# Kernel tuning notes

Hardware: AMD Instinct MI355X
Metric: run time of the kernel (lower is better)

## Reference

```python
import jax, jax.numpy as jnp
import numpy as np

B, T, D = 4, 4096, 1024
C = 8.0  # RG_LRU constant c
LOGIT_LO = float(np.log(0.9 / 0.1))    # logit(0.9)
LOGIT_HI = float(np.log(0.999 / 0.001))  # logit(0.999)


def setup_inputs() -> dict:
    key = jax.random.key(0)
    ks = jax.random.split(key, 12)
    s = 1.0 / np.sqrt(D)
    z = lambda: jnp.zeros((D,), jnp.float32)
    return {
        "x": jax.random.normal(ks[0], (B, T, D), jnp.float32),
        "g1": jnp.ones((D,), jnp.float32),
        "g2": jnp.ones((D,), jnp.float32),
        # RecurrentBlock: shared linear, kernel-1 conv, output linear
        "W_lin": jax.random.normal(ks[1], (D, D), jnp.float32) * s, "b_lin": z(),
        "W_conv": jax.random.normal(ks[2], (D, D), jnp.float32) * s, "b_conv": z(),
        "W_lin2": jax.random.normal(ks[3], (D, D), jnp.float32) * s, "b_lin2": z(),
        # RG_LRU params
        "Wa": jax.random.normal(ks[4], (D, D), jnp.float32) * s, "ba": z(),
        "Wx": jax.random.normal(ks[5], (D, D), jnp.float32) * s, "bx": z(),
        "Lam": jax.random.uniform(ks[6], (D,), jnp.float32, LOGIT_LO, LOGIT_HI),
        # GatedMLPBlock
        "W1": jax.random.normal(ks[7], (D, D), jnp.float32) * s, "b1": z(),
        "W2": jax.random.normal(ks[8], (D, D), jnp.float32) * s, "b2": z(),
        "W3": jax.random.normal(ks[9], (D, D), jnp.float32) * s, "b3": z(),
    }


def rms_norm(x, g):
    # F.normalize(x, dim=-1) * sqrt(d) * g
    n = jnp.maximum(jnp.linalg.norm(x, axis=-1, keepdims=True), 1e-12)
    return (x / n) * (x.shape[-1] ** 0.5) * g


def rg_lru(x, Wa, ba, Wx, bx, Lam):
    # x: [B, T, D]
    rt = jax.nn.sigmoid(jnp.einsum('btd,hd->bth', x, Wa) + ba)
    it = jax.nn.sigmoid(jnp.einsum('btd,hd->bth', x, Wx) + bx)
    log_a = -jax.nn.softplus(-Lam)          # [D]
    a = jnp.exp(log_a * rt / C)             # [B, T, D]
    gated = jnp.sqrt(1.0 - a * a) * (it * x)

    def step(h, ag):
        at, gt = ag
        h = at * h + gt
        return h, h

    h0 = jnp.zeros((x.shape[0], x.shape[2]), x.dtype)
    _, hs = jax.lax.scan(step, h0, (jnp.swapaxes(a, 0, 1), jnp.swapaxes(gated, 0, 1)))
    return jnp.swapaxes(hs, 0, 1)           # [B, T, D]


def reference(x, g1, g2, W_lin, b_lin, W_conv, b_conv, W_lin2, b_lin2,
              Wa, ba, Wx, bx, Lam, W1, b1, W2, b2, W3, b3):
    residual = x
    xn = rms_norm(x, g1)

    # RecurrentBlock (note: same linear used for both branches, as in source)
    lin = xn @ W_lin.T + b_lin
    x_gel = jax.nn.gelu(lin, approximate=False)
    x_rg = lin @ W_conv.T + b_conv          # Conv1d kernel_size=1 == pointwise linear
    x_rg = rg_lru(x_rg, Wa, ba, Wx, bx, Lam)
    xr = (x_gel * x_rg) @ W_lin2.T + b_lin2

    residual = xr + residual
    xm = rms_norm(residual, g2)

    # GatedMLPBlock
    out = jax.nn.sigmoid(xm @ W1.T + b1)
    gate = jax.nn.gelu(out, approximate=False)
    combined = gate * (xm @ W2.T + b2)
    y = combined @ W3.T + b3
    return y + residual
```

## Files before the change

kernel.cpp:

```cpp
#include <hip/hip_runtime.h>
#include <cstdint>
#include <cstddef>

typedef unsigned short u16;
typedef __attribute__((ext_vector_type(8))) __bf16 bf16x8;
typedef __attribute__((ext_vector_type(4))) float f32x4;

#define DD 1024
#define MM 16384
#define NCH 64
#define CLEN 64

__device__ __forceinline__ u16 f2b(float f) {
    uint32_t u = __float_as_uint(f);
    u += 0x7fffu + ((u >> 16) & 1u);
    return (u16)(u >> 16);
}
__device__ __forceinline__ float b2f(u16 v) {
    return __uint_as_float(((uint32_t)v) << 16);
}
__device__ __forceinline__ float sigmoid_f(float v) { return 1.f / (1.f + __expf(-v)); }
__device__ __forceinline__ float gelu_f(float v) {
    return 0.5f * v * (1.f + erff(v * 0.70710678118654752f));
}

__device__ __forceinline__ void glds16(const u16* g, u16* l) {
    __builtin_amdgcn_global_load_lds(
        (const __attribute__((address_space(1))) void*)g,
        (__attribute__((address_space(3))) void*)l, 16, 0, 0);
}

template <int MODE>
__global__ __launch_bounds__(256, 2)
void gemm_bt(const u16* __restrict__ A, const u16* __restrict__ Bw,
             const float* __restrict__ bias,
             const float* __restrict__ auxf, const u16* __restrict__ auxb,
             u16* __restrict__ outb, float* __restrict__ outf)
{
    const int K = DD, N = DD;
    __shared__ __align__(16) u16 As[128 * 32];
    __shared__ __align__(16) u16 Bs[128 * 32];

    const int tid = threadIdx.x;
    const int m0 = blockIdx.y * 128, n0 = blockIdx.x * 128;
    const int wave = tid >> 6, lane = tid & 63;
    const int wm = (wave >> 1) * 64, wn = (wave & 1) * 64;
    const int lr = lane & 15, lq = lane >> 4;

    const u16* Ag = A + (size_t)(m0 + (tid >> 2)) * K + (tid & 3) * 8;
    const u16* Bg = Bw + (size_t)(n0 + (tid >> 2)) * K + (tid & 3) * 8;
    u16* la0 = &As[tid * 8];
    u16* la1 = &As[(tid + 256) * 8];
    u16* lb0 = &Bs[tid * 8];
    u16* lb1 = &Bs[(tid + 256) * 8];

    f32x4 acc[4][4] = {};

    for (int k0 = 0; k0 < K; k0 += 32) {
        glds16(Ag + k0, la0);
        glds16(Ag + (size_t)64 * K + k0, la1);
        glds16(Bg + k0, lb0);
        glds16(Bg + (size_t)64 * K + k0, lb1);
        __syncthreads();

        bf16x8 av[4], bv[4];
#pragma unroll
        for (int i = 0; i < 4; i++)
            av[i] = *(const bf16x8*)&As[(wm + i * 16 + lr) * 32 + lq * 8];
#pragma unroll
        for (int j = 0; j < 4; j++)
            bv[j] = *(const bf16x8*)&Bs[(wn + j * 16 + lr) * 32 + lq * 8];
#pragma unroll
        for (int i = 0; i < 4; i++)
#pragma unroll
            for (int j = 0; j < 4; j++)
                acc[i][j] = __builtin_amdgcn_mfma_f32_16x16x32_bf16(
                    av[i], bv[j], acc[i][j], 0, 0, 0);
        __syncthreads();
    }

#pragma unroll
    for (int i = 0; i < 4; i++) {
        const int mrow = m0 + wm + i * 16 + lq * 4;
#pragma unroll
        for (int j = 0; j < 4; j++) {
            const int ncol = n0 + wn + j * 16 + lr;
            const float bz = bias[ncol];
#pragma unroll
            for (int p = 0; p < 4; p++) {
                const size_t idx = (size_t)(mrow + p) * N + ncol;
                float v = acc[i][j][p] + bz;
                if constexpr (MODE == 0) {
                    outb[idx] = f2b(v);
                } else if constexpr (MODE == 1) {
                    outb[idx] = f2b(sigmoid_f(v));
                } else if constexpr (MODE == 2) {
                    outf[idx] = v + auxf[idx];
                } else if constexpr (MODE == 3) {
                    outb[idx] = f2b(gelu_f(sigmoid_f(v)));
                } else if constexpr (MODE == 4) {
                    outb[idx] = f2b(b2f(auxb[idx]) * v);
                } else {
                    outf[idx] = v + auxf[idx];
                }
            }
        }
    }
}

__global__ __launch_bounds__(256)
void rmsnorm_k(const float* __restrict__ x, const float* __restrict__ g,
               u16* __restrict__ out)
{
    const int row = blockIdx.x;
    const int t = threadIdx.x;
    const float4 v = ((const float4*)(x + (size_t)row * DD))[t];
    float ss = v.x * v.x + v.y * v.y + v.z * v.z + v.w * v.w;
#pragma unroll
    for (int o = 32; o > 0; o >>= 1) ss += __shfl_down(ss, o, 64);
    __shared__ float wsum[4];
    if ((t & 63) == 0) wsum[t >> 6] = ss;
    __syncthreads();
    const float tot = wsum[0] + wsum[1] + wsum[2] + wsum[3];
    const float sc = 32.0f * rsqrtf(fmaxf(tot, 1e-24f));
    const float4 gv = ((const float4*)g)[t];
    ushort4 o4;
    o4.x = f2b(v.x * sc * gv.x);
    o4.y = f2b(v.y * sc * gv.y);
    o4.z = f2b(v.z * sc * gv.z);
    o4.w = f2b(v.w * sc * gv.w);
    ((ushort4*)(out + (size_t)row * DD))[t] = o4;
}

__global__ __launch_bounds__(256)
void conv_w(const float* __restrict__ in, u16* __restrict__ out)
{
    const int i = (blockIdx.x * 256 + threadIdx.x) * 4;
    const float4 v = *(const float4*)(in + i);
    ushort4 o;
    o.x = f2b(v.x); o.y = f2b(v.y); o.z = f2b(v.z); o.w = f2b(v.w);
    *(ushort4*)(out + i) = o;
}

__global__ __launch_bounds__(256)
void scan_chunks(const u16* __restrict__ rt, const u16* __restrict__ it,
                 const u16* __restrict__ rg, const float* __restrict__ Lam,
                 float* __restrict__ P, float* __restrict__ Hl)
{
    const int d = blockIdx.x * 256 + threadIdx.x;
    const int c = blockIdx.y, b = blockIdx.z;
    const float k = -log1pf(__expf(-Lam[d])) * 0.125f;
    const size_t base = (((size_t)b * 4096) + (size_t)c * CLEN) * DD + d;
    float p = 1.f, h = 0.f;
#pragma unroll 4
    for (int t = 0; t < CLEN; t++) {
        const size_t ix = base + (size_t)t * DD;
        const float r = b2f(rt[ix]);
        const float i = b2f(it[ix]);
        const float xv = b2f(rg[ix]);
        const float a = __expf(k * r);
        const float g = sqrtf(fmaxf(1.f - a * a, 0.f)) * (i * xv);
        p *= a;
        h = fmaf(a, h, g);
    }
    const int o = (b * NCH + c) * DD + d;
    P[o] = p;
    Hl[o] = h;
}

__global__ __launch_bounds__(256)
void scan_carry(const float* __restrict__ P, const float* __restrict__ Hl,
                float* __restrict__ Cin)
{
    const int idx = blockIdx.x * 256 + threadIdx.x;
    const int b = idx >> 10, d = idx & 1023;
    float h = 0.f;
    for (int c = 0; c < NCH; c++) {
        const int o = (b * NCH + c) * DD + d;
        Cin[o] = h;
        h = fmaf(P[o], h, Hl[o]);
    }
}

__global__ __launch_bounds__(256)
void scan_apply(const u16* __restrict__ rt, const u16* __restrict__ it,
                const u16* __restrict__ rg, const u16* __restrict__ lin,
                const float* __restrict__ Lam, const float* __restrict__ Cin,
                u16* __restrict__ yin)
{
    const int d = blockIdx.x * 256 + threadIdx.x;
    const int c = blockIdx.y, b = blockIdx.z;
    const float k = -log1pf(__expf(-Lam[d])) * 0.125f;
    const size_t base = (((size_t)b * 4096) + (size_t)c * CLEN) * DD + d;
    float h = Cin[(b * NCH + c) * DD + d];
#pragma unroll 4
    for (int t = 0; t < CLEN; t++) {
        const size_t ix = base + (size_t)t * DD;
        const float r = b2f(rt[ix]);
        const float i = b2f(it[ix]);
        const float xv = b2f(rg[ix]);
        const float a = __expf(k * r);
        const float g = sqrtf(fmaxf(1.f - a * a, 0.f)) * (i * xv);
        h = fmaf(a, h, g);
        const float l = b2f(lin[ix]);
        yin[ix] = f2b(gelu_f(l) * h);
    }
}

extern "C" void kernel_launch(void* const* d_in, const int* in_sizes, int n_in,
                              void* d_out, int out_size, void* d_ws, size_t ws_size,
                              hipStream_t stream)
{
    const float* x      = (const float*)d_in[0];
    const float* g1     = (const float*)d_in[1];
    const float* g2     = (const float*)d_in[2];
    const float* W_lin  = (const float*)d_in[3];
    const float* b_lin  = (const float*)d_in[4];
    const float* W_conv = (const float*)d_in[5];
    const float* b_conv = (const float*)d_in[6];
    const float* W_lin2 = (const float*)d_in[7];
    const float* b_lin2 = (const float*)d_in[8];
    const float* Wa     = (const float*)d_in[9];
    const float* ba     = (const float*)d_in[10];
    const float* Wx     = (const float*)d_in[11];
    const float* bx     = (const float*)d_in[12];
    const float* Lam    = (const float*)d_in[13];
    const float* W1     = (const float*)d_in[14];
    const float* b1     = (const float*)d_in[15];
    const float* W2     = (const float*)d_in[16];
    const float* b2     = (const float*)d_in[17];
    const float* W3     = (const float*)d_in[18];
    const float* b3     = (const float*)d_in[19];
    float* out = (float*)d_out;

    char* p = (char*)d_ws;
    auto alloc = [&](size_t bytes) -> char* {
        char* q = p;
        p += (bytes + 255) & ~(size_t)255;
        return q;
    };
    const size_t MD = (size_t)MM * DD;
    u16* wbf[8];
    for (int i = 0; i < 8; i++) wbf[i] = (u16*)alloc((size_t)DD * DD * 2);
    u16* t0 = (u16*)alloc(MD * 2);
    u16* t1 = (u16*)alloc(MD * 2);
    u16* t2 = (u16*)alloc(MD * 2);
    u16* t3 = (u16*)alloc(MD * 2);
    u16* t4 = (u16*)alloc(MD * 2);
    float* res2 = (float*)alloc(MD * 4);
    float* P   = (float*)alloc((size_t)4 * NCH * DD * 4);
    float* Hl  = (float*)alloc((size_t)4 * NCH * DD * 4);
    float* Cin = (float*)alloc((size_t)4 * NCH * DD * 4);

    const float* wsrc[8] = {W_lin, W_conv, Wa, Wx, W_lin2, W1, W2, W3};
    for (int i = 0; i < 8; i++)
        conv_w<<<(DD * DD) / 1024, 256, 0, stream>>>(wsrc[i], wbf[i]);

    const dim3 gg(DD / 128, MM / 128);
    const dim3 sg(DD / 256, NCH, 4);

    rmsnorm_k<<<MM, 256, 0, stream>>>(x, g1, t0);
    gemm_bt<0><<<gg, 256, 0, stream>>>(t0, wbf[0], b_lin, nullptr, nullptr, t1, nullptr);
    gemm_bt<0><<<gg, 256, 0, stream>>>(t1, wbf[1], b_conv, nullptr, nullptr, t2, nullptr);
    gemm_bt<1><<<gg, 256, 0, stream>>>(t2, wbf[2], ba, nullptr, nullptr, t0, nullptr);
    gemm_bt<1><<<gg, 256, 0, stream>>>(t2, wbf[3], bx, nullptr, nullptr, t3, nullptr);
    scan_chunks<<<sg, 256, 0, stream>>>(t0, t3, t2, Lam, P, Hl);
    scan_carry<<<4096 / 256, 256, 0, stream>>>(P, Hl, Cin);
    scan_apply<<<sg, 256, 0, stream>>>(t0, t3, t2, t1, Lam, Cin, t4);
    gemm_bt<2><<<gg, 256, 0, stream>>>(t4, wbf[4], b_lin2, x, nullptr, nullptr, res2);
    rmsnorm_k<<<MM, 256, 0, stream>>>(res2, g2, t0);
    gemm_bt<3><<<gg, 256, 0, stream>>>(t0, wbf[5], b1, nullptr, nullptr, t1, nullptr);
    gemm_bt<4><<<gg, 256, 0, stream>>>(t0, wbf[6], b2, nullptr, t1, t2, nullptr);
    gemm_bt<5><<<gg, 256, 0, stream>>>(t2, wbf[7], b3, res2, nullptr, nullptr, out);
}
```

Measured before the change: 711.7 us.

## Fuse paired GEMMs, swizzle LDS and tile order, stage bf16 epilogues through LDS

Two GEMMs that read the same input (Wa/Wx gates, and W1/W2 in the MLP) are merged into one dual-B kernel, so the A tile is loaded once and the intermediate gate tensor no longer goes through global memory. The LDS layout gets an XOR swizzle on the k-chunk to reduce bank conflicts. A 1D grid with grouped tile ordering improves L2 reuse. The bf16 epilogues are staged through padded LDS so global stores are coalesced 16-byte writes, and the eight weight-conversion launches become one. The dual kernel doubles accumulator registers, which may lower occupancy.

Result: faster. 654.6 us (-8.0%).

```diff
diff --git a/kernel.cpp b/kernel.cpp
--- a/kernel.cpp
+++ b/kernel.cpp
@@ -10,6 +10,7 @@
 #define MM 16384
 #define NCH 64
 #define CLEN 64
+#define EPAD 136
 
 __device__ __forceinline__ u16 f2b(float f) {
     uint32_t u = __float_as_uint(f);
@@ -30,29 +31,38 @@
         (__attribute__((address_space(3))) void*)l, 16, 0, 0);
 }
 
+__device__ __forceinline__ void swiz(int l, int& mt, int& nt) {
+    const int g = l >> 6, r = l & 63;
+    mt = g * 8 + (r & 7);
+    nt = r >> 3;
+}
+
 template <int MODE>
 __global__ __launch_bounds__(256, 2)
 void gemm_bt(const u16* __restrict__ A, const u16* __restrict__ Bw,
-             const float* __restrict__ bias,
-             const float* __restrict__ auxf, const u16* __restrict__ auxb,
+             const float* __restrict__ bias, const float* __restrict__ auxf,
              u16* __restrict__ outb, float* __restrict__ outf)
 {
     const int K = DD, N = DD;
-    __shared__ __align__(16) u16 As[128 * 32];
-    __shared__ __align__(16) u16 Bs[128 * 32];
-
+    __shared__ __align__(16) u16 smem[8704];
+    u16* As = smem;
+    u16* Bs = smem + 4096;
+
+    int mt, nt; swiz(blockIdx.x, mt, nt);
+    const int m0 = mt * 128, n0 = nt * 128;
     const int tid = threadIdx.x;
-    const int m0 = blockIdx.y * 128, n0 = blockIdx.x * 128;
     const int wave = tid >> 6, lane = tid & 63;
     const int wm = (wave >> 1) * 64, wn = (wave & 1) * 64;
     const int lr = lane & 15, lq = lane >> 4;
 
-    const u16* Ag = A + (size_t)(m0 + (tid >> 2)) * K + (tid & 3) * 8;
-    const u16* Bg = Bw + (size_t)(n0 + (tid >> 2)) * K + (tid & 3) * 8;
+    const int trow = tid >> 2, tcol = tid & 3;
+    const int kswz = (tcol ^ ((trow >> 1) & 3)) * 8;
+    const u16* Ag = A + (size_t)(m0 + trow) * K + kswz;
+    const u16* Bg = Bw + (size_t)(n0 + trow) * K + kswz;
     u16* la0 = &As[tid * 8];
-    u16* la1 = &As[(tid + 256) * 8];
+    u16* la1 = &As[tid * 8 + 2048];
     u16* lb0 = &Bs[tid * 8];
-    u16* lb1 = &Bs[(tid + 256) * 8];
+    u16* lb1 = &Bs[tid * 8 + 2048];
 
     f32x4 acc[4][4] = {};
 
@@ -64,12 +74,13 @@
         __syncthreads();
 
         bf16x8 av[4], bv[4];
+        const int cs = (lq ^ ((lr >> 1) & 3)) * 8;
 #pragma unroll
         for (int i = 0; i < 4; i++)
-            av[i] = *(const bf16x8*)&As[(wm + i * 16 + lr) * 32 + lq * 8];
+            av[i] = *(const bf16x8*)&As[(wm + i * 16 + lr) * 32 + cs];
 #pragma unroll
         for (int j = 0; j < 4; j++)
-            bv[j] = *(const bf16x8*)&Bs[(wn + j * 16 + lr) * 32 + lq * 8];
+            bv[j] = *(const bf16x8*)&Bs[(wn + j * 16 + lr) * 32 + cs];
 #pragma unroll
         for (int i = 0; i < 4; i++)
 #pragma unroll
@@ -79,30 +90,171 @@
         __syncthreads();
     }
 
-#pragma unroll
-    for (int i = 0; i < 4; i++) {
-        const int mrow = m0 + wm + i * 16 + lq * 4;
+    if constexpr (MODE == 0) {
+        for (int half = 0; half < 2; half++) {
+            __syncthreads();
+            if (wm == half * 64) {
+#pragma unroll
+                for (int i = 0; i < 4; i++)
+#pragma unroll
+                    for (int j = 0; j < 4; j++) {
+                        const int col = wn + j * 16 + lr;
+                        const float bz = bias[n0 + col];
+#pragma unroll
+                        for (int p = 0; p < 4; p++)
+                            smem[(i * 16 + lq * 4 + p) * EPAD + col] =
+                                f2b(acc[i][j][p] + bz);
+                    }
+            }
+            __syncthreads();
+#pragma unroll
+            for (int t = 0; t < 4; t++) {
+                const int f = t * 256 + tid;
+                const int row = f >> 4, c8 = (f & 15) * 8;
+                *(uint4*)&outb[(size_t)(m0 + half * 64 + row) * N + n0 + c8] =
+                    *(const uint4*)&smem[row * EPAD + c8];
+            }
+        }
+    } else {
+#pragma unroll
+        for (int i = 0; i < 4; i++) {
+            const int mrow = m0 + wm + i * 16 + lq * 4;
+#pragma unroll
+            for (int j = 0; j < 4; j++) {
+                const int ncol = n0 + wn + j * 16 + lr;
+                const float bz = bias[ncol];
+#pragma unroll
+                for (int p = 0; p < 4; p++) {
+                    const size_t idx = (size_t)(mrow + p) * N + ncol;
+                    outf[idx] = acc[i][j][p] + bz + auxf[idx];
+                }
+            }
+        }
+    }
+}
+
+template <int DMODE>
+__global__ __launch_bounds__(256, 2)
+void gemm_dual(const u16* __restrict__ A, const u16* __restrict__ B1,
+               const u16* __restrict__ B2,
+               const float* __restrict__ bias1, const float* __restrict__ bias2,
+               u16* __restrict__ out1, u16* __restrict__ out2)
+{
+    const int K = DD, N = DD;
+    __shared__ __align__(16) u16 smem[12288];
+    u16* As = smem;
+    u16* Bs1 = smem + 4096;
+    u16* Bs2 = smem + 8192;
+
+    int mt, nt; swiz(blockIdx.x, mt, nt);
+    const int m0 = mt * 128, n0 = nt * 128;
+    const int tid = threadIdx.x;
+    const int wave = tid >> 6, lane = tid & 63;
+    const int wm = (wave >> 1) * 64, wn = (wave & 1) * 64;
+    const int lr = lane & 15, lq = lane >> 4;
+
+    const int trow = tid >> 2, tcol = tid & 3;
+    const int kswz = (tcol ^ ((trow >> 1) & 3)) * 8;
+    const u16* Ag  = A  + (size_t)(m0 + trow) * K + kswz;
+    const u16* B1g = B1 + (size_t)(n0 + trow) * K + kswz;
+    const u16* B2g = B2 + (size_t)(n0 + trow) * K + kswz;
+    u16* la0 = &As[tid * 8];
+    u16* la1 = &As[tid * 8 + 2048];
+    u16* lb10 = &Bs1[tid * 8];
+    u16* lb11 = &Bs1[tid * 8 + 2048];
+    u16* lb20 = &Bs2[tid * 8];
+    u16* lb21 = &Bs2[tid * 8 + 2048];
+
+    f32x4 acc1[4][4] = {}, acc2[4][4] = {};
+
+    for (int k0 = 0; k0 < K; k0 += 32) {
+        glds16(Ag + k0, la0);
+        glds16(Ag + (size_t)64 * K + k0, la1);
+        glds16(B1g + k0, lb10);
+        glds16(B1g + (size_t)64 * K + k0, lb11);
+        glds16(B2g + k0, lb20);
+        glds16(B2g + (size_t)64 * K + k0, lb21);
+        __syncthreads();
+
+        bf16x8 av[4], bv1[4], bv2[4];
+        const int cs = (lq ^ ((lr >> 1) & 3)) * 8;
+#pragma unroll
+        for (int i = 0; i < 4; i++)
+            av[i] = *(const bf16x8*)&As[(wm + i * 16 + lr) * 32 + cs];
 #pragma unroll
         for (int j = 0; j < 4; j++) {
-            const int ncol = n0 + wn + j * 16 + lr;
-            const float bz = bias[ncol];
-#pragma unroll
-            for (int p = 0; p < 4; p++) {
-                const size_t idx = (size_t)(mrow + p) * N + ncol;
-                float v = acc[i][j][p] + bz;
-                if constexpr (MODE == 0) {
-                    outb[idx] = f2b(v);
-                } else if constexpr (MODE == 1) {
-                    outb[idx] = f2b(sigmoid_f(v));
-                } else if constexpr (MODE == 2) {
-                    outf[idx] = v + auxf[idx];
-                } else if constexpr (MODE == 3) {
-                    outb[idx] = f2b(gelu_f(sigmoid_f(v)));
-                } else if constexpr (MODE == 4) {
-                    outb[idx] = f2b(b2f(auxb[idx]) * v);
-                } else {
-                    outf[idx] = v + auxf[idx];
+            bv1[j] = *(const bf16x8*)&Bs1[(wn + j * 16 + lr) * 32 + cs];
+            bv2[j] = *(const bf16x8*)&Bs2[(wn + j * 16 + lr) * 32 + cs];
+        }
+#pragma unroll
+        for (int i = 0; i < 4; i++)
+#pragma unroll
+            for (int j = 0; j < 4; j++) {
+                acc1[i][j] = __builtin_amdgcn_mfma_f32_16x16x32_bf16(
+                    av[i], bv1[j], acc1[i][j], 0, 0, 0);
+                acc2[i][j] = __builtin_amdgcn_mfma_f32_16x16x32_bf16(
+                    av[i], bv2[j], acc2[i][j], 0, 0, 0);
+            }
+        __syncthreads();
+    }
+
+    if constexpr (DMODE == 0) {
+#pragma unroll
+        for (int o = 0; o < 2; o++) {
+            const float* bz = o ? bias2 : bias1;
+            u16* op = o ? out2 : out1;
+            for (int half = 0; half < 2; half++) {
+                __syncthreads();
+                if (wm == half * 64) {
+#pragma unroll
+                    for (int i = 0; i < 4; i++)
+#pragma unroll
+                        for (int j = 0; j < 4; j++) {
+                            const int col = wn + j * 16 + lr;
+                            const float bb = bz[n0 + col];
+#pragma unroll
+                            for (int p = 0; p < 4; p++) {
+                                const float v = (o ? acc2[i][j][p] : acc1[i][j][p]) + bb;
+                                smem[(i * 16 + lq * 4 + p) * EPAD + col] = f2b(sigmoid_f(v));
+                            }
+                        }
                 }
+                __syncthreads();
+#pragma unroll
+                for (int t = 0; t < 4; t++) {
+                    const int f = t * 256 + tid;
+                    const int row = f >> 4, c8 = (f & 15) * 8;
+                    *(uint4*)&op[(size_t)(m0 + half * 64 + row) * N + n0 + c8] =
+                        *(const uint4*)&smem[row * EPAD + c8];
+                }
+            }
+        }
+    } else {
+        for (int half = 0; half < 2; half++) {
+            __syncthreads();
+            if (wm == half * 64) {
+#pragma unroll
+                for (int i = 0; i < 4; i++)
+#pragma unroll
+                    for (int j = 0; j < 4; j++) {
+                        const int col = wn + j * 16 + lr;
+                        const float bb1 = bias1[n0 + col];
+                        const float bb2 = bias2[n0 + col];
+#pragma unroll
+                        for (int p = 0; p < 4; p++) {
+                            const float g = gelu_f(sigmoid_f(acc1[i][j][p] + bb1));
+                            smem[(i * 16 + lq * 4 + p) * EPAD + col] =
+                                f2b(g * (acc2[i][j][p] + bb2));
+                        }
+                    }
+            }
+            __syncthreads();
+#pragma unroll
+            for (int t = 0; t < 4; t++) {
+                const int f = t * 256 + tid;
+                const int row = f >> 4, c8 = (f & 15) * 8;
+                *(uint4*)&out1[(size_t)(m0 + half * 64 + row) * N + n0 + c8] =
+                    *(const uint4*)&smem[row * EPAD + c8];
             }
         }
     }
@@ -132,14 +284,17 @@
     ((ushort4*)(out + (size_t)row * DD))[t] = o4;
 }
 
+struct W8 { const float* s[8]; };
 __global__ __launch_bounds__(256)
-void conv_w(const float* __restrict__ in, u16* __restrict__ out)
-{
+void conv_w8(W8 w, u16* __restrict__ out)
+{
+    const float* in = w.s[blockIdx.y];
+    u16* o = out + (size_t)blockIdx.y * DD * DD;
     const int i = (blockIdx.x * 256 + threadIdx.x) * 4;
     const float4 v = *(const float4*)(in + i);
-    ushort4 o;
-    o.x = f2b(v.x); o.y = f2b(v.y); o.z = f2b(v.z); o.w = f2b(v.w);
-    *(ushort4*)(out + i) = o;
+    ushort4 r;
+    r.x = f2b(v.x); r.y = f2b(v.y); r.z = f2b(v.z); r.w = f2b(v.w);
+    *(ushort4*)(o + i) = r;
 }
 
 __global__ __launch_bounds__(256)
@@ -240,8 +395,7 @@
         return q;
     };
     const size_t MD = (size_t)MM * DD;
-    u16* wbf[8];
-    for (int i = 0; i < 8; i++) wbf[i] = (u16*)alloc((size_t)DD * DD * 2);
+    u16* wball = (u16*)alloc((size_t)8 * DD * DD * 2);
     u16* t0 = (u16*)alloc(MD * 2);
     u16* t1 = (u16*)alloc(MD * 2);
     u16* t2 = (u16*)alloc(MD * 2);
@@ -252,24 +406,25 @@
     float* Hl  = (float*)alloc((size_t)4 * NCH * DD * 4);
     float* Cin = (float*)alloc((size_t)4 * NCH * DD * 4);
 
-    const float* wsrc[8] = {W_lin, W_conv, Wa, Wx, W_lin2, W1, W2, W3};
-    for (int i = 0; i < 8; i++)
-        conv_w<<<(DD * DD) / 1024, 256, 0, stream>>>(wsrc[i], wbf[i]);
-
-    const dim3 gg(DD / 128, MM / 128);
+    W8 w8;
+    w8.s[0] = W_lin; w8.s[1] = W_conv; w8.s[2] = Wa; w8.s[3] = Wx;
+    w8.s[4] = W_lin2; w8.s[5] = W1; w8.s[6] = W2; w8.s[7] = W3;
+    conv_w8<<<dim3(DD * DD / 1024, 8), 256, 0, stream>>>(w8, wball);
+    u16* wbf[8];
+    for (int i = 0; i < 8; i++) wbf[i] = wball + (size_t)i * DD * DD;
+
+    const int gg = (MM / 128) * (DD / 128);
     const dim3 sg(DD / 256, NCH, 4);
 
     rmsnorm_k<<<MM, 256, 0, stream>>>(x, g1, t0);
-    gemm_bt<0><<<gg, 256, 0, stream>>>(t0, wbf[0], b_lin, nullptr, nullptr, t1, nullptr);
-    gemm_bt<0><<<gg, 256, 0, stream>>>(t1, wbf[1], b_conv, nullptr, nullptr, t2, nullptr);
-    gemm_bt<1><<<gg, 256, 0, stream>>>(t2, wbf[2], ba, nullptr, nullptr, t0, nullptr);
-    gemm_bt<1><<<gg, 256, 0, stream>>>(t2, wbf[3], bx, nullptr, nullptr, t3, nullptr);
+    gemm_bt<0><<<gg, 256, 0, stream>>>(t0, wbf[0], b_lin, nullptr, t1, nullptr);
+    gemm_bt<0><<<gg, 256, 0, stream>>>(t1, wbf[1], b_conv, nullptr, t2, nullptr);
+    gemm_dual<0><<<gg, 256, 0, stream>>>(t2, wbf[2], wbf[3], ba, bx, t0, t3);
     scan_chunks<<<sg, 256, 0, stream>>>(t0, t3, t2, Lam, P, Hl);
     scan_carry<<<4096 / 256, 256, 0, stream>>>(P, Hl, Cin);
     scan_apply<<<sg, 256, 0, stream>>>(t0, t3, t2, t1, Lam, Cin, t4);
-    gemm_bt<2><<<gg, 256, 0, stream>>>(t4, wbf[4], b_lin2, x, nullptr, nullptr, res2);
+    gemm_bt<2><<<gg, 256, 0, stream>>>(t4, wbf[4], b_lin2, x, nullptr, res2);
     rmsnorm_k<<<MM, 256, 0, stream>>>(res2, g2, t0);
-    gemm_bt<3><<<gg, 256, 0, stream>>>(t0, wbf[5], b1, nullptr, nullptr, t1, nullptr);
-    gemm_bt<4><<<gg, 256, 0, stream>>>(t0, wbf[6], b2, nullptr, t1, t2, nullptr);
-    gemm_bt<5><<<gg, 256, 0, stream>>>(t2, wbf[7], b3, res2, nullptr, nullptr, out);
-}
+    gemm_dual<1><<<gg, 256, 0, stream>>>(t0, wbf[5], wbf[6], b1, b2, t2, nullptr);
+    gemm_bt<2><<<gg, 256, 0, stream>>>(t2, wbf[7], b3, res2, nullptr, out);
+}
```
